# Optimization experiments

Measured on AMD Instinct MI355X. Metric: run time of the kernel, lower is better.

## Reference

```python
import jax, jax.numpy as jnp
import numpy as np

B, T, D = 2, 2048, 2048
H, HKV, DH = 16, 4, 128  # n_heads, n_kv_heads, d_head
EPS = 1e-6


def _rms_norm(t):
    # normalize over last dim, no learned weight (matches F.rms_norm default)
    return t * jax.lax.rsqrt(jnp.mean(t * t, axis=-1, keepdims=True) + EPS)


def _ortho_rope(t, cos, sin):
    # t: (b, h, t, d); unfold(-1,2,2) -> even/odd pairs
    x0 = t[..., 0::2]  # (b,h,t,d/2)
    x1 = t[..., 1::2]
    y0 = x0 * cos - x1 * sin
    y1 = x1 * cos + x0 * sin
    # NOTE: concatenated halves (NOT re-interleaved), faithful to source
    return jnp.concatenate((y0, y1), axis=-1)


def setup_inputs() -> dict:
    key = jax.random.key(0)
    ks = jax.random.split(key, 10)
    return {
        "x": jax.random.normal(ks[0], (B, T, D), jnp.float32),
        "pos_ids": jnp.broadcast_to(jnp.arange(T, dtype=jnp.int64), (B, T)),
        "cos": jax.random.normal(ks[1], (T, DH // 2), jnp.float32),
        "sin": jax.random.normal(ks[2], (T, DH // 2), jnp.float32),
        "v1": jax.random.normal(ks[3], (B, HKV, T, DH), jnp.float32),
        "Wq": jax.random.normal(ks[4], (H * DH, D), jnp.float32) * (D ** -0.5),
        "Wk": jax.random.normal(ks[5], (HKV * DH, D), jnp.float32) * (D ** -0.5),
        "Wv": jax.random.normal(ks[6], (HKV * DH, D), jnp.float32) * (D ** -0.5),
        "Wo": jax.random.normal(ks[7], (D, D), jnp.float32) * (D ** -0.5),
        "gate_w": jax.random.normal(ks[8], (H, H), jnp.float32) * 0.1,
        "v_lamb": jnp.float32(0.5),
    }


def reference(x, pos_ids, cos, sin, v1, Wq, Wk, Wv, Wo, gate_w, v_lamb):
    b, t, _ = x.shape
    # fused QKV projections (Linear, no bias: x @ W.T), split to heads
    q = (x @ Wq.T).reshape(b, t, H, DH).transpose(0, 2, 1, 3)    # (b,H,t,d)
    k = (x @ Wk.T).reshape(b, t, HKV, DH).transpose(0, 2, 1, 3)  # (b,Hkv,t,d)
    v = (x @ Wv.T).reshape(b, t, HKV, DH).transpose(0, 2, 1, 3)
    # value residual: lerp(v, v1, lamb) = v + lamb*(v1 - v)
    v = v + v_lamb * (v1 - v)
    # QK RMSNorm then ortho RoPE
    q = _ortho_rope(_rms_norm(q), cos, sin)
    k = _ortho_rope(_rms_norm(k), cos, sin)
    # kv_cache.upsert modeled as prefill: k,v unchanged, causal block mask
    g = H // HKV  # GQA group size
    k = jnp.repeat(k, g, axis=1)  # (b,H,t,d)
    vfull = jnp.repeat(v, g, axis=1)
    scale = DH ** -0.5
    scores = jnp.einsum('bhqd,bhkd->bhqk', q, k) * scale
    causal = jnp.tril(jnp.ones((t, t), dtype=bool))
    scores = jnp.where(causal, scores, jnp.finfo(scores.dtype).min)
    attn = jax.nn.softmax(scores, axis=-1)
    y = jnp.einsum('bhqk,bhkd->bhqd', attn, vfull)  # (b,H,t,d)
    # per-head sigmoid gate from first n_heads channels of x
    gates = jax.nn.sigmoid(x[..., :H] @ gate_w.T)   # (b,t,H)
    y = y * gates.transpose(0, 2, 1)[..., None]     # (b,H,t,1)
    y = y.transpose(0, 2, 1, 3).reshape(b, t, H * DH)
    out = y @ Wo.T
    return (out, v1)
```

## Files before the change

kernel.cpp:

```cpp
#include <hip/hip_runtime.h>

typedef __bf16 bf16;
typedef __attribute__((ext_vector_type(8))) __bf16 bf16x8;
typedef __attribute__((ext_vector_type(4))) __bf16 bf16x4;
typedef __attribute__((ext_vector_type(4))) float f32x4;
typedef __attribute__((ext_vector_type(4))) short short4v;
typedef __attribute__((ext_vector_type(4))) unsigned int u32x4;

#define BB 2
#define TT 2048
#define DD 2048
#define HH 16
#define HKV 4
#define DHD 128
#define NQKV 3072

__device__ __forceinline__ void gl_lds16(const bf16* g, bf16* l) {
    __builtin_amdgcn_global_load_lds(
        (const __attribute__((address_space(1))) void*)g,
        (__attribute__((address_space(3))) void*)l, 16, 0, 0);
}

__device__ __forceinline__ f32x4 mfma16bf16(short4v a, short4v b, f32x4 c) {
#if defined(__HIP_DEVICE_COMPILE__)
    return __builtin_amdgcn_mfma_f32_16x16x16bf16_1k(a, b, c, 0, 0, 0);
#else
    return c;
#endif
}

__global__ void cvt_bf16(const float* __restrict__ src, bf16* __restrict__ dst, int n8) {
    int i = blockIdx.x * 256 + threadIdx.x;
    if (i >= n8) return;
    float4 a = ((const float4*)src)[i * 2];
    float4 b = ((const float4*)src)[i * 2 + 1];
    bf16x8 v;
    v[0] = (bf16)a.x; v[1] = (bf16)a.y; v[2] = (bf16)a.z; v[3] = (bf16)a.w;
    v[4] = (bf16)b.x; v[5] = (bf16)b.y; v[6] = (bf16)b.z; v[7] = (bf16)b.w;
    *(bf16x8*)(dst + (size_t)i * 8) = v;
}

template <int MODE>
__global__ void gemm_bt(const bf16* __restrict__ A, const bf16* __restrict__ Bw,
                        int M, int N, int K,
                        float* __restrict__ Cout,
                        bf16* __restrict__ qb, bf16* __restrict__ kb,
                        bf16* __restrict__ vtb,
                        const float* __restrict__ v1,
                        const float* __restrict__ cosb,
                        const float* __restrict__ sinb,
                        const float* __restrict__ lamp) {
    constexpr int SMEM_ELE = (MODE == 1) ? 17920 : 16384;
    __shared__ bf16 smem[SMEM_ELE];
    bf16* As = smem;
    bf16* Bs = smem + 8192;
    const int tid = threadIdx.x;
    const int w = tid >> 6, lane = tid & 63;
    const int l15 = lane & 15, quad = lane >> 4;
    const int m0 = blockIdx.y * 128, n0 = blockIdx.x * 128;
    const int wm = (w & 1) * 64, wn = (w >> 1) * 64;

    f32x4 acc[4][4] = {};
    const int lrow = lane >> 2;
    const int lcol = (lane & 3) * 8;

    for (int k0 = 0; k0 < K; k0 += 64) {
#pragma unroll
        for (int i = 0; i < 4; i++) {
            int c = w * 4 + i;
            int kc2 = c >> 3, rc = c & 7;
            int row = rc * 16 + lrow;
            int kk = k0 + kc2 * 32 + lcol;
            gl_lds16(A + (size_t)(m0 + row) * K + kk, As + c * 512);
            gl_lds16(Bw + (size_t)(n0 + row) * K + kk, Bs + c * 512);
        }
        __syncthreads();
#pragma unroll
        for (int kc2 = 0; kc2 < 2; kc2++) {
            bf16x8 af[4], bfr[4];
#pragma unroll
            for (int mi = 0; mi < 4; mi++)
                af[mi] = *(const bf16x8*)(As + kc2 * 4096 + ((wm >> 4) + mi) * 512 + l15 * 32 + quad * 8);
#pragma unroll
            for (int ni = 0; ni < 4; ni++)
                bfr[ni] = *(const bf16x8*)(Bs + kc2 * 4096 + ((wn >> 4) + ni) * 512 + l15 * 32 + quad * 8);
#pragma unroll
            for (int mi = 0; mi < 4; mi++)
#pragma unroll
                for (int ni = 0; ni < 4; ni++)
                    acc[mi][ni] = __builtin_amdgcn_mfma_f32_16x16x32_bf16(af[mi], bfr[ni], acc[mi][ni], 0, 0, 0);
        }
        __syncthreads();
    }

    if constexpr (MODE == 0) {
#pragma unroll
        for (int mi = 0; mi < 4; mi++)
#pragma unroll
            for (int ni = 0; ni < 4; ni++)
#pragma unroll
                for (int r = 0; r < 4; r++) {
                    int m = m0 + wm + mi * 16 + quad * 4 + r;
                    int n = n0 + wn + ni * 16 + l15;
                    Cout[(size_t)m * N + n] = acc[mi][ni][r];
                }
    } else {
        const int hid = n0 >> 7;
        const int b = m0 >> 11;
        const int t0 = m0 & (TT - 1);
        bf16* ep = smem;

        if (hid < 20) {
            float* ssum = (float*)(smem + 17408);
            float ssq[4][4];
#pragma unroll
            for (int mi = 0; mi < 4; mi++)
#pragma unroll
                for (int r = 0; r < 4; r++) {
                    float s = 0.f;
#pragma unroll
                    for (int ni = 0; ni < 4; ni++) {
                        float v = acc[mi][ni][r];
                        s += v * v;
                    }
                    s += __shfl_xor(s, 1);
                    s += __shfl_xor(s, 2);
                    s += __shfl_xor(s, 4);
                    s += __shfl_xor(s, 8);
                    ssq[mi][r] = s;
                }
            if (l15 == 0) {
#pragma unroll
                for (int mi = 0; mi < 4; mi++)
#pragma unroll
                    for (int r = 0; r < 4; r++)
                        ssum[(wn >> 6) * 128 + wm + mi * 16 + quad * 4 + r] = ssq[mi][r];
            }
            __syncthreads();
            const float QSCALE = 0.08838834764831845f * 1.4426950408889634f;
            float rn[4][4];
#pragma unroll
            for (int mi = 0; mi < 4; mi++)
#pragma unroll
                for (int r = 0; r < 4; r++) {
                    int row = wm + mi * 16 + quad * 4 + r;
                    float ss = ssum[row] + ssum[128 + row];
                    float rv = rsqrtf(ss * (1.f / 128.f) + 1e-6f);
                    if (hid < HH) rv *= QSCALE;
                    rn[mi][r] = rv;
                }
#pragma unroll
            for (int mi = 0; mi < 4; mi++)
#pragma unroll
                for (int ni = 0; ni < 4; ni++)
#pragma unroll
                    for (int r = 0; r < 4; r++) {
                        float sv = acc[mi][ni][r] * rn[mi][r];
                        float pv = __shfl_xor(sv, 1);
                        int nl = wn + ni * 16 + l15;
                        int j = nl >> 1;
                        int tl = wm + mi * 16 + quad * 4 + r;
                        float c = cosb[(size_t)(t0 + tl) * 64 + j];
                        float s = sinb[(size_t)(t0 + tl) * 64 + j];
                        float o = (nl & 1) ? (sv * c + pv * s) : (sv * c - pv * s);
                        int oc = (nl & 1) ? (64 + j) : j;
                        ep[tl * 136 + oc] = (bf16)o;
                    }
            __syncthreads();
            bf16* dst = (hid < HH)
                ? (qb + ((size_t)(b * HH + hid) * TT + t0) * DHD)
                : (kb + ((size_t)(b * HKV + (hid - HH)) * TT + t0) * DHD);
            int tl = tid >> 1, half = tid & 1;
#pragma unroll
            for (int c8 = 0; c8 < 8; c8++)
                *(bf16x8*)(dst + (size_t)tl * DHD + half * 64 + c8 * 8) =
                    *(const bf16x8*)(ep + tl * 136 + half * 64 + c8 * 8);
        } else {
            float lam = lamp[0];
            int vh = hid - 20;
            const float* v1b = v1 + ((size_t)(b * HKV + vh) * TT) * DHD;
#pragma unroll
            for (int mi = 0; mi < 4; mi++)
#pragma unroll
                for (int ni = 0; ni < 4; ni++)
#pragma unroll
                    for (int r = 0; r < 4; r++) {
                        int d = wn + ni * 16 + l15;
                        int tl = wm + mi * 16 + quad * 4 + r;
                        float val = acc[mi][ni][r];
                        float vm = val + lam * (v1b[(size_t)(t0 + tl) * DHD + d] - val);
                        ep[d * 136 + tl] = (bf16)vm;
                    }
            __syncthreads();
            bf16* dstv = vtb + ((size_t)(b * HKV + vh) * DHD) * TT + t0;
            int dd = tid >> 1, half = tid & 1;
#pragma unroll
            for (int c8 = 0; c8 < 8; c8++)
                *(bf16x8*)(dstv + (size_t)dd * TT + half * 64 + c8 * 8) =
                    *(const bf16x8*)(ep + dd * 136 + half * 64 + c8 * 8);
        }
    }
}

__global__ void gatesk(const float* __restrict__ x, const float* __restrict__ gw,
                       float* __restrict__ gates) {
    __shared__ float gws[256];
    gws[threadIdx.x] = gw[threadIdx.x];
    __syncthreads();
    int idx = blockIdx.x * 256 + threadIdx.x;
    int h = idx & 15, token = idx >> 4;
    const float* xr = x + (size_t)token * DD;
    float z = 0.f;
#pragma unroll
    for (int j = 0; j < 16; j++) z += xr[j] * gws[h * 16 + j];
    gates[idx] = 1.f / (1.f + __expf(-z));
}

__global__ __launch_bounds__(512, 2) void fattn(const bf16* __restrict__ qbuf,
                                                const bf16* __restrict__ kbuf,
                                                const bf16* __restrict__ vt,
                                                const float* __restrict__ gates,
                                                bf16* __restrict__ yb) {
    __shared__ bf16 Ks[2][4 * 2048];
    __shared__ bf16 VTs[2][4 * 2048];

    const int bid = blockIdx.x;
    const int bh = bid & 31;
    const int g = bid >> 5;
    const int h = bh & 15, b = bh >> 4;
    const int hk = h >> 2;
    const int tid = threadIdx.x, w = tid >> 6, lane = tid & 63;
    const int wq = w & 3, grp = w >> 2;
    const int l15 = lane & 15, quad = lane >> 4;

    const bf16* qbase = qbuf + ((size_t)(b * HH + h) * TT) * DHD;
    const bf16* kbase = kbuf + ((size_t)(b * HKV + hk) * TT) * DHD;
    const bf16* vtbase = vt + ((size_t)(b * HKV + hk) * DHD) * TT;

    const int Tq0 = grp ? (15 - g) : g;
    const int Tq1 = grp ? (16 + g) : (31 - g);
    const int ktmax_blk = 31 - g;

    bf16x8 qf0[4], qf1[4];
#pragma unroll
    for (int kc = 0; kc < 4; kc++) {
        qf0[kc] = *(const bf16x8*)(qbase + (size_t)(Tq0 * 64 + wq * 16 + l15) * DHD + kc * 32 + quad * 8);
        qf1[kc] = *(const bf16x8*)(qbase + (size_t)(Tq1 * 64 + wq * 16 + l15) * DHD + kc * 32 + quad * 8);
    }

    bool dm[4][4];
#pragma unroll
    for (int ni = 0; ni < 4; ni++)
#pragma unroll
        for (int r = 0; r < 4; r++)
            dm[ni][r] = (ni * 16 + quad * 4 + r) > (wq * 16 + l15);

    const int srow = lane >> 2;
    const int scg = (((lane & 3) ^ ((lane >> 3) & 3)) * 8);
    const int vd = lane >> 1;
    const int vh = (((lane & 1) ^ ((lane >> 3) & 1)) * 8);

    auto stage = [&](int kt, int buf) {
        if (grp == 0) {
#pragma unroll
            for (int i = 0; i < 4; i++)
                gl_lds16(kbase + (size_t)(kt * 64 + wq * 16 + srow) * DHD + i * 32 + scg,
                         &Ks[buf][i * 2048 + wq * 512]);
        } else {
#pragma unroll
            for (int i = 0; i < 4; i++)
                gl_lds16(vtbase + (size_t)(wq * 32 + vd) * TT + kt * 64 + i * 16 + vh,
                         &VTs[buf][i * 2048 + wq * 512]);
        }
    };

    stage(0, 0);

    f32x4 O0[8] = {}, O1[8] = {};
    float m0 = -INFINITY, l0 = 0.f, m1 = -INFINITY, l1 = 0.f;

    for (int kt = 0; kt <= ktmax_blk; kt++) {
        int cur = kt & 1;
        __syncthreads();
        if (kt < ktmax_blk) stage(kt + 1, cur ^ 1);

        if (kt > Tq1) continue;
        const bool a0 = (kt <= Tq0);

        f32x4 s0[4], s1[4];
#pragma unroll
        for (int ni = 0; ni < 4; ni++) {
            bf16x8 kfl[4];
#pragma unroll
            for (int kc = 0; kc < 4; kc++)
                kfl[kc] = *(const bf16x8*)(&Ks[cur][kc * 2048 + (ni * 16 + l15) * 32 +
                                                   ((quad ^ ((l15 >> 1) & 3)) * 8)]);
            f32x4 z1 = {};
#pragma unroll
            for (int kc = 0; kc < 4; kc++)
                z1 = __builtin_amdgcn_mfma_f32_16x16x32_bf16(kfl[kc], qf1[kc], z1, 0, 0, 0);
            s1[ni] = z1;
            if (a0) {
                f32x4 z0 = {};
#pragma unroll
                for (int kc = 0; kc < 4; kc++)
                    z0 = __builtin_amdgcn_mfma_f32_16x16x32_bf16(kfl[kc], qf0[kc], z0, 0, 0, 0);
                s0[ni] = z0;
            }
        }

        short4v bp0[4], bp1[4];
        {
            if (kt == Tq1) {
#pragma unroll
                for (int ni = 0; ni < 4; ni++)
#pragma unroll
                    for (int r = 0; r < 4; r++)
                        if (dm[ni][r]) s1[ni][r] = -INFINITY;
            }
            float mx = s1[0][0];
#pragma unroll
            for (int ni = 0; ni < 4; ni++)
#pragma unroll
                for (int r = 0; r < 4; r++) mx = fmaxf(mx, s1[ni][r]);
            mx = fmaxf(mx, __shfl_xor(mx, 16));
            mx = fmaxf(mx, __shfl_xor(mx, 32));
            float mold = m1;
            bool noresc = __all(mx <= mold + 8.f);
            float mnew = noresc ? mold : fmaxf(mold, mx);
            float rs = 0.f;
#pragma unroll
            for (int ni = 0; ni < 4; ni++) {
                union { bf16x4 hv; short4v sv4; } u;
#pragma unroll
                for (int r = 0; r < 4; r++) {
                    float pe = __builtin_amdgcn_exp2f(s1[ni][r] - mnew);
                    u.hv[r] = (bf16)pe;
                    rs += pe;
                }
                bp1[ni] = u.sv4;
            }
            rs += __shfl_xor(rs, 16);
            rs += __shfl_xor(rs, 32);
            if (!noresc) {
                float al = __builtin_amdgcn_exp2f(mold - mnew);
                l1 *= al;
#pragma unroll
                for (int dn = 0; dn < 8; dn++)
#pragma unroll
                    for (int r = 0; r < 4; r++) O1[dn][r] *= al;
                m1 = mnew;
            }
            l1 += rs;
        }
        if (a0) {
            if (kt == Tq0) {
#pragma unroll
                for (int ni = 0; ni < 4; ni++)
#pragma unroll
                    for (int r = 0; r < 4; r++)
                        if (dm[ni][r]) s0[ni][r] = -INFINITY;
            }
            float mx = s0[0][0];
#pragma unroll
            for (int ni = 0; ni < 4; ni++)
#pragma unroll
                for (int r = 0; r < 4; r++) mx = fmaxf(mx, s0[ni][r]);
            mx = fmaxf(mx, __shfl_xor(mx, 16));
            mx = fmaxf(mx, __shfl_xor(mx, 32));
            float mold = m0;
            bool noresc = __all(mx <= mold + 8.f);
            float mnew = noresc ? mold : fmaxf(mold, mx);
            float rs = 0.f;
#pragma unroll
            for (int ni = 0; ni < 4; ni++) {
                union { bf16x4 hv; short4v sv4; } u;
#pragma unroll
                for (int r = 0; r < 4; r++) {
                    float pe = __builtin_amdgcn_exp2f(s0[ni][r] - mnew);
                    u.hv[r] = (bf16)pe;
                    rs += pe;
                }
                bp0[ni] = u.sv4;
            }
            rs += __shfl_xor(rs, 16);
            rs += __shfl_xor(rs, 32);
            if (!noresc) {
                float al = __builtin_amdgcn_exp2f(mold - mnew);
                l0 *= al;
#pragma unroll
                for (int dn = 0; dn < 8; dn++)
#pragma unroll
                    for (int r = 0; r < 4; r++) O0[dn][r] *= al;
                m0 = mnew;
            }
            l0 += rs;
        }

#pragma unroll
        for (int ni = 0; ni < 4; ni++) {
            short4v vfl[8];
#pragma unroll
            for (int dn = 0; dn < 8; dn++)
                vfl[dn] = *(const short4v*)(&VTs[cur][ni * 2048 + (dn * 16 + l15) * 16 +
                                                     ((quad ^ (((l15 >> 2) & 1) << 1)) * 4)]);
#pragma unroll
            for (int dn = 0; dn < 8; dn++)
                O1[dn] = mfma16bf16(vfl[dn], bp1[ni], O1[dn]);
            if (a0) {
#pragma unroll
                for (int dn = 0; dn < 8; dn++)
                    O0[dn] = mfma16bf16(vfl[dn], bp0[ni], O0[dn]);
            }
        }
    }

    auto epi = [&](const f32x4* Oc, float lsum, int qt) {
        int qg = qt * 64 + wq * 16 + l15;
        float gi = gates[((size_t)b * TT + qg) * HH + h] / lsum;
#pragma unroll
        for (int dn = 0; dn < 8; dn++) {
            bf16x4 o;
#pragma unroll
            for (int r = 0; r < 4; r++) o[r] = (bf16)(Oc[dn][r] * gi);
            *(bf16x4*)(yb + ((size_t)(b * TT + qg) * HH + h) * DHD + dn * 16 + quad * 4) = o;
        }
    };
    epi(O0, l0, Tq0);
    epi(O1, l1, Tq1);
}

extern "C" void kernel_launch(void* const* d_in, const int* in_sizes, int n_in,
                              void* d_out, int out_size, void* d_ws, size_t ws_size,
                              hipStream_t stream) {
    const float* x    = (const float*)d_in[0];
    const float* cosb = (const float*)d_in[2];
    const float* sinb = (const float*)d_in[3];
    const float* v1   = (const float*)d_in[4];
    const float* Wq   = (const float*)d_in[5];
    const float* Wk   = (const float*)d_in[6];
    const float* Wv   = (const float*)d_in[7];
    const float* Wo   = (const float*)d_in[8];
    const float* gw   = (const float*)d_in[9];
    const float* lam  = (const float*)d_in[10];
    float* out = (float*)d_out;

    char* ws = (char*)d_ws;
    bf16* xb     = (bf16*)(ws);
    bf16* wqkvb  = (bf16*)(ws + 16777216);
    bf16* wob    = (bf16*)(ws + 29360128);
    bf16* qb     = (bf16*)(ws + 79691776);
    bf16* kb     = (bf16*)(ws + 96468992);
    bf16* vtb    = (bf16*)(ws + 100663296);
    float* gts   = (float*)(ws + 104857600);
    bf16* yb     = xb;

    cvt_bf16<<<4096, 256, 0, stream>>>(x, xb, 1048576);
    cvt_bf16<<<2048, 256, 0, stream>>>(Wq, wqkvb, 524288);
    cvt_bf16<<<512, 256, 0, stream>>>(Wk, wqkvb + 4194304, 131072);
    cvt_bf16<<<512, 256, 0, stream>>>(Wv, wqkvb + 5242880, 131072);
    cvt_bf16<<<2048, 256, 0, stream>>>(Wo, wob, 524288);

    gemm_bt<1><<<dim3(24, 32), 256, 0, stream>>>(xb, wqkvb, 4096, NQKV, 2048,
                                                 nullptr, qb, kb, vtb, v1,
                                                 cosb, sinb, lam);
    gatesk<<<256, 256, 0, stream>>>(x, gw, gts);
    fattn<<<256, 512, 0, stream>>>(qb, kb, vtb, gts, yb);
    gemm_bt<0><<<dim3(16, 32), 256, 0, stream>>>(yb, wob, 4096, 2048, 2048,
                                                 out, nullptr, nullptr, nullptr,
                                                 nullptr, nullptr, nullptr, nullptr);
    (void)hipMemcpyAsync(out + 8388608, v1, (size_t)2097152 * sizeof(float),
                         hipMemcpyDeviceToDevice, stream);
}
```

Baseline: 326.5 us.

## Use 16x16x32 bf16 MFMA for PV product with re-laid-out V tiles

```diff
diff --git a/kernel.cpp b/kernel.cpp
--- a/kernel.cpp
+++ b/kernel.cpp
@@ -19,14 +19,6 @@
     __builtin_amdgcn_global_load_lds(
         (const __attribute__((address_space(1))) void*)g,
         (__attribute__((address_space(3))) void*)l, 16, 0, 0);
-}
-
-__device__ __forceinline__ f32x4 mfma16bf16(short4v a, short4v b, f32x4 c) {
-#if defined(__HIP_DEVICE_COMPILE__)
-    return __builtin_amdgcn_mfma_f32_16x16x16bf16_1k(a, b, c, 0, 0, 0);
-#else
-    return c;
-#endif
 }
 
 __global__ void cvt_bf16(const float* __restrict__ src, bf16* __restrict__ dst, int n8) {
@@ -222,7 +214,7 @@
                                                 const float* __restrict__ gates,
                                                 bf16* __restrict__ yb) {
     __shared__ bf16 Ks[2][4 * 2048];
-    __shared__ bf16 VTs[2][4 * 2048];
+    __shared__ bf16 VTs[2][8192];
 
     const int bid = blockIdx.x;
     const int bh = bid & 31;
@@ -253,12 +245,13 @@
     for (int ni = 0; ni < 4; ni++)
 #pragma unroll
         for (int r = 0; r < 4; r++)
-            dm[ni][r] = (ni * 16 + quad * 4 + r) > (wq * 16 + l15);
+            dm[ni][r] = ((ni >> 1) * 32 + quad * 8 + (ni & 1) * 4 + r) > (wq * 16 + l15);
 
     const int srow = lane >> 2;
-    const int scg = (((lane & 3) ^ ((lane >> 3) & 3)) * 8);
-    const int vd = lane >> 1;
-    const int vh = (((lane & 1) ^ ((lane >> 3) & 1)) * 8);
+    const int gst = (((lane >> 5) & 1) << 1) | ((lane >> 3) & 1);
+    const int scg = ((lane & 3) ^ gst) * 8;
+    const int vrow = lane >> 3;
+    const int vcg = ((lane & 7) ^ ((lane >> 3) & 7)) * 8;
 
     auto stage = [&](int kt, int buf) {
         if (grp == 0) {
@@ -269,15 +262,19 @@
         } else {
 #pragma unroll
             for (int i = 0; i < 4; i++)
-                gl_lds16(vtbase + (size_t)(wq * 32 + vd) * TT + kt * 64 + i * 16 + vh,
-                         &VTs[buf][i * 2048 + wq * 512]);
+                gl_lds16(vtbase + (size_t)(wq * 32 + i * 8 + vrow) * TT + kt * 64 + vcg,
+                         &VTs[buf][wq * 2048 + i * 512]);
         }
     };
 
     stage(0, 0);
+
+    const int gk = (((l15 >> 2) & 1) << 1) | ((l15 >> 1) & 1);
 
     f32x4 O0[8] = {}, O1[8] = {};
     float m0 = -INFINITY, l0 = 0.f, m1 = -INFINITY, l1 = 0.f;
+
+    union PW { bf16x4 h[2]; bf16x8 v; };
 
     for (int kt = 0; kt <= ktmax_blk; kt++) {
         int cur = kt & 1;
@@ -288,13 +285,14 @@
         const bool a0 = (kt <= Tq0);
 
         f32x4 s0[4], s1[4];
+        __builtin_amdgcn_s_setprio(1);
 #pragma unroll
         for (int ni = 0; ni < 4; ni++) {
+            int rr = (ni >> 1) * 32 + (l15 >> 2) * 8 + (ni & 1) * 4 + (l15 & 3);
             bf16x8 kfl[4];
 #pragma unroll
             for (int kc = 0; kc < 4; kc++)
-                kfl[kc] = *(const bf16x8*)(&Ks[cur][kc * 2048 + (ni * 16 + l15) * 32 +
-                                                   ((quad ^ ((l15 >> 1) & 3)) * 8)]);
+                kfl[kc] = *(const bf16x8*)(&Ks[cur][kc * 2048 + rr * 32 + ((quad ^ gk) * 8)]);
             f32x4 z1 = {};
 #pragma unroll
             for (int kc = 0; kc < 4; kc++)
@@ -308,8 +306,9 @@
                 s0[ni] = z0;
             }
         }
-
-        short4v bp0[4], bp1[4];
+        __builtin_amdgcn_s_setprio(0);
+
+        PW pw0[2], pw1[2];
         {
             if (kt == Tq1) {
 #pragma unroll
@@ -331,14 +330,14 @@
             float rs = 0.f;
 #pragma unroll
             for (int ni = 0; ni < 4; ni++) {
-                union { bf16x4 hv; short4v sv4; } u;
+                bf16x4 hv;
 #pragma unroll
                 for (int r = 0; r < 4; r++) {
                     float pe = __builtin_amdgcn_exp2f(s1[ni][r] - mnew);
-                    u.hv[r] = (bf16)pe;
+                    hv[r] = (bf16)pe;
                     rs += pe;
                 }
-                bp1[ni] = u.sv4;
+                pw1[ni >> 1].h[ni & 1] = hv;
             }
             rs += __shfl_xor(rs, 16);
             rs += __shfl_xor(rs, 32);
@@ -374,14 +373,14 @@
             float rs = 0.f;
 #pragma unroll
             for (int ni = 0; ni < 4; ni++) {
-                union { bf16x4 hv; short4v sv4; } u;
+                bf16x4 hv;
 #pragma unroll
                 for (int r = 0; r < 4; r++) {
                     float pe = __builtin_amdgcn_exp2f(s0[ni][r] - mnew);
-                    u.hv[r] = (bf16)pe;
+                    hv[r] = (bf16)pe;
                     rs += pe;
                 }
-                bp0[ni] = u.sv4;
+                pw0[ni >> 1].h[ni & 1] = hv;
             }
             rs += __shfl_xor(rs, 16);
             rs += __shfl_xor(rs, 32);
@@ -397,22 +396,24 @@
             l0 += rs;
         }
 
-#pragma unroll
-        for (int ni = 0; ni < 4; ni++) {
-            short4v vfl[8];
+        __builtin_amdgcn_s_setprio(1);
+#pragma unroll
+        for (int ni2 = 0; ni2 < 2; ni2++) {
+            bf16x8 vfl[8];
 #pragma unroll
             for (int dn = 0; dn < 8; dn++)
-                vfl[dn] = *(const short4v*)(&VTs[cur][ni * 2048 + (dn * 16 + l15) * 16 +
-                                                     ((quad ^ (((l15 >> 2) & 1) << 1)) * 4)]);
+                vfl[dn] = *(const bf16x8*)(&VTs[cur][(dn * 16 + l15) * 64 +
+                                                    (((ni2 * 4 + quad) ^ (l15 & 7)) * 8)]);
 #pragma unroll
             for (int dn = 0; dn < 8; dn++)
-                O1[dn] = mfma16bf16(vfl[dn], bp1[ni], O1[dn]);
+                O1[dn] = __builtin_amdgcn_mfma_f32_16x16x32_bf16(vfl[dn], pw1[ni2].v, O1[dn], 0, 0, 0);
             if (a0) {
 #pragma unroll
                 for (int dn = 0; dn < 8; dn++)
-                    O0[dn] = mfma16bf16(vfl[dn], bp0[ni], O0[dn]);
-            }
-        }
+                    O0[dn] = __builtin_amdgcn_mfma_f32_16x16x32_bf16(vfl[dn], pw0[ni2].v, O0[dn], 0, 0, 0);
+            }
+        }
+        __builtin_amdgcn_s_setprio(0);
     }
 
     auto epi = [&](const f32x4* Oc, float lsum, int qt) {
```

Measured after the change: 312.9 us. 1.04x faster.
